# Kernel tuning notes

Measured on AMD Instinct MI355X. Metric: run time of the kernel, lower is better.

The kernel has to match this reference:

```python
import jax, jax.numpy as jnp
import numpy as np

B, T, D, K = 32, 2048, 1024, 31


def setup_inputs() -> dict:
    key = jax.random.key(0)
    ks = jax.random.split(key, 8)
    query = jax.random.normal(ks[0], (B, D), dtype=jnp.float32)
    memory = jax.random.normal(ks[1], (B, T, D), dtype=jnp.float32)
    prev_attn = jax.nn.softmax(jax.random.normal(ks[2], (B, T)), axis=-1).astype(jnp.float32)
    cum_attn = jax.random.uniform(ks[3], (B, T), dtype=jnp.float32)
    mask = jax.random.bernoulli(ks[4], 0.2, (B, T))
    mask = mask.at[:, 0].set(False)  # keep at least one valid position per row
    scale = 0.02
    Wq = jax.random.normal(ks[5], (D, D), dtype=jnp.float32) * scale    # torch Linear weight [out,in]
    Wm = jax.random.normal(ks[6], (D, D), dtype=jnp.float32) * scale
    k2 = jax.random.split(ks[7], 2)
    Wloc = jax.random.normal(k2[0], (D, 2, K), dtype=jnp.float32) * scale  # Conv1d weight [out_ch,in_ch,k]
    v = jax.random.normal(k2[1], (D,), dtype=jnp.float32) * scale          # Linear(d_model,1) weight squeezed
    return {"query": query, "memory": memory, "prev_attn": prev_attn,
            "cum_attn": cum_attn, "mask": mask,
            "Wq": Wq, "Wm": Wm, "Wloc": Wloc, "v": v}


def reference(query, memory, prev_attn, cum_attn, mask, Wq, Wm, Wloc, v):
    pad = Wloc.shape[-1] // 2
    # location features: [B,2,T] conv -> [B,D,T] -> [B,T,D]
    loc_in = jnp.stack([prev_attn, cum_attn], axis=1)
    loc = jax.lax.conv_general_dilated(
        loc_in, Wloc, window_strides=(1,), padding=[(pad, pad)],
        dimension_numbers=("NCW", "OIW", "NCW"))
    loc = jnp.transpose(loc, (0, 2, 1))                 # [B,T,D]
    q = (query @ Wq.T)[:, None, :]                      # [B,1,D]
    m = jnp.einsum("btd,ed->bte", memory, Wm)           # [B,T,D]
    e = jnp.einsum("btd,d->bt", jnp.tanh(q + m + loc), v)  # [B,T]
    e = jnp.where(mask, -jnp.inf, e)
    a = jax.nn.softmax(e, axis=1)                       # [B,T]
    ctx = jnp.einsum("bt,btd->bd", a, memory)           # [B,D]
    return ctx, a
```

## Files before the change

kernel.cpp:

```cpp
#include <hip/hip_runtime.h>
#include <math.h>

#define BATCH 32
#define T 2048
#define D 1024
#define KW 31
#define CPAD 15
#define KEXT 62
#define KTOT 1088
#define BM 256
#define BN 256
#define KSTEP 64
#define NK (KTOT / KSTEP)

typedef __bf16 bf16_8 __attribute__((ext_vector_type(8)));
typedef __bf16 bf16_4 __attribute__((ext_vector_type(4)));
typedef float  f32x4  __attribute__((ext_vector_type(4)));

__device__ __forceinline__ float tanh_fast(float x) {
    return 1.f - 2.f * __builtin_amdgcn_rcpf(__expf(2.f * x) + 1.f);
}

__device__ __forceinline__ void glds16(const void* gsrc, void* ldst) {
    __builtin_amdgcn_global_load_lds(
        (const __attribute__((address_space(1))) unsigned int*)gsrc,
        (__attribute__((address_space(3))) unsigned int*)ldst, 16, 0, 0);
}

#define VM6 asm volatile("s_waitcnt vmcnt(6)" ::: "memory")
#define VM4 asm volatile("s_waitcnt vmcnt(4)" ::: "memory")
#define VM0 asm volatile("s_waitcnt vmcnt(0)" ::: "memory")
#define BAR __builtin_amdgcn_s_barrier()
#define PRIO1 __builtin_amdgcn_s_setprio(1)
#define PRIO0 __builtin_amdgcn_s_setprio(0)

#define PREP_BLOCKS 17472
__global__ __launch_bounds__(256) void k_prep_all(
    const float* __restrict__ Wm, const float* __restrict__ Wloc,
    __bf16* __restrict__ Bext,
    const float* __restrict__ memory, __bf16* __restrict__ Amem,
    const float* __restrict__ prev, const float* __restrict__ cum,
    const float* __restrict__ query, const float* __restrict__ Wq,
    float* __restrict__ qout) {
    const int gb = blockIdx.x;
    if (gb < 4096) {
        const int nvec = BATCH * T * (D / 16);
        for (int idx = gb * 256 + threadIdx.x; idx < nvec; idx += 4096 * 256) {
            const int row = idx >> 6;
            const int c = (idx & 63) * 16;
            const float* src = memory + (size_t)row * D + c;
            const f32x4 a0 = *(const f32x4*)(src);
            const f32x4 a1 = *(const f32x4*)(src + 4);
            const f32x4 a2 = *(const f32x4*)(src + 8);
            const f32x4 a3 = *(const f32x4*)(src + 12);
            bf16_8 o0, o1;
            #pragma unroll
            for (int u = 0; u < 4; ++u) {
                o0[u] = (__bf16)a0[u]; o0[u + 4] = (__bf16)a1[u];
                o1[u] = (__bf16)a2[u]; o1[u + 4] = (__bf16)a3[u];
            }
            __bf16* dst = Amem + (size_t)row * KTOT + c;
            *(bf16_8*)(dst) = o0;
            *(bf16_8*)(dst + 8) = o1;
        }
    } else if (gb < 12288) {
        const int j = gb - 4096;
        const int xb = j & 255;
        const int b = j >> 8;
        const int w = threadIdx.x >> 6;
        const int lane = threadIdx.x & 63;
        const int d = xb * 4 + w;
        const float* qrow = query + (size_t)b * D;
        const float* wrow = Wq + (size_t)d * D;
        float s = 0.f;
        #pragma unroll
        for (int i = 0; i < D / 64; ++i) s += qrow[lane + i * 64] * wrow[lane + i * 64];
        #pragma unroll
        for (int off = 32; off > 0; off >>= 1) s += __shfl_down(s, off, 64);
        if (lane == 0) qout[(size_t)b * D + d] = s;
    } else if (gb < 16384) {
        const int idx = (gb - 12288) * 256 + threadIdx.x;
        const int row = idx >> 4;
        const int j0 = (idx & 15) * 4;
        const int b = row >> 11;
        const int t = row & (T - 1);
        bf16_4 o;
        #pragma unroll
        for (int u = 0; u < 4; ++u) {
            const int jj = j0 + u;
            float val = 0.f;
            if (jj < KEXT) {
                const int c = (jj >= KW) ? 1 : 0;
                const int kp = jj - c * KW;
                const int ts = t + kp - CPAD;
                if (ts >= 0 && ts < T)
                    val = (c ? cum : prev)[(size_t)b * T + ts];
            }
            o[u] = (__bf16)val;
        }
        *(bf16_4*)(Amem + (size_t)row * KTOT + D + j0) = o;
    } else {
        const int idx = (gb - 16384) * 256 + threadIdx.x;
        const int d = idx / (KTOT / 4);
        const int kk = (idx % (KTOT / 4)) * 4;
        bf16_4 o;
        #pragma unroll
        for (int u = 0; u < 4; ++u) {
            const int k = kk + u;
            float val = 0.f;
            if (k < D) val = Wm[(size_t)d * D + k];
            else {
                const int jj = k - D;
                if (jj < KEXT) {
                    const int c = (jj >= KW) ? 1 : 0;
                    const int kp = jj - c * KW;
                    val = Wloc[((size_t)d * 2 + c) * KW + kp];
                }
            }
            o[u] = (__bf16)val;
        }
        *(bf16_4*)(Bext + (size_t)d * KTOT + kk) = o;
    }
}

__global__ __launch_bounds__(512, 2) void k_gemm_e(
    const __bf16* __restrict__ Amem, const __bf16* __restrict__ Bext,
    const float* __restrict__ qv, const float* __restrict__ vvec,
    float* __restrict__ e_part) {
    __shared__ bf16_8 As[2][2048];
    __shared__ bf16_8 Bs[2][2048];

    const int t0 = blockIdx.x * BM;
    const int d0 = blockIdx.y * BN;
    const int b  = blockIdx.z;
    const int tid  = threadIdx.x;
    const int lane = tid & 63;
    const int w    = tid >> 6;
    const int wm   = w >> 2;
    const int wn   = w & 3;
    const int ml   = lane & 15;
    const int qk   = lane >> 4;

    f32x4 acc[8][4] = {};

    const __bf16* gA[2][2];
    const __bf16* gB[2][2];
    int sA[2][2], sB[2][2];
    #pragma unroll
    for (int h = 0; h < 2; ++h) {
        #pragma unroll
        for (int j = 0; j < 2; ++j) {
            const int idx = j * 8 + w;
            const int p = idx >> 1, kfa = idx & 1;
            const int mf = h * 4 + (p & 3) + (idx & 8);
            const int nf = h * 2 + (p & 1) + (p >> 1) * 4;
            gA[h][j] = Amem + ((size_t)b * T + t0 + mf * 16 + ml) * KTOT + kfa * 32 + qk * 8;
            sA[h][j] = (mf * 2 + kfa) * 64;
            gB[h][j] = Bext + (size_t)(d0 + nf * 16 + ml) * KTOT + kfa * 32 + qk * 8;
            sB[h][j] = (nf * 2 + kfa) * 64;
        }
    }

    bf16_8 areg[4][2];
    bf16_8 breg0[2][2], breg1[2][2];

    auto STG_A = [&](int h, int kcol, bf16_8* dst) {
        glds16(gA[h][0] + kcol, dst + sA[h][0]);
        glds16(gA[h][1] + kcol, dst + sA[h][1]);
    };
    auto STG_B = [&](int h, int kcol, bf16_8* dst) {
        glds16(gB[h][0] + kcol, dst + sB[h][0]);
        glds16(gB[h][1] + kcol, dst + sB[h][1]);
    };
    auto LDA = [&](const bf16_8* buf, int ih) {
        #pragma unroll
        for (int i = 0; i < 4; ++i)
            #pragma unroll
            for (int kf = 0; kf < 2; ++kf)
                areg[i][kf] = buf[((wm * 8 + ih * 4 + i) * 2 + kf) * 64 + lane];
    };
    auto LDB = [&](bf16_8 (&dst)[2][2], const bf16_8* buf, int jh) {
        #pragma unroll
        for (int j = 0; j < 2; ++j)
            #pragma unroll
            for (int kf = 0; kf < 2; ++kf)
                dst[j][kf] = buf[((wn * 4 + jh * 2 + j) * 2 + kf) * 64 + lane];
    };
    auto QMM = [&](bf16_8 (&bb)[2][2], int ih, int jh) {
        #pragma unroll
        for (int i = 0; i < 4; ++i)
            #pragma unroll
            for (int kf = 0; kf < 2; ++kf)
                #pragma unroll
                for (int j = 0; j < 2; ++j)
                    acc[ih * 4 + i][jh * 2 + j] = __builtin_amdgcn_mfma_f32_16x16x32_bf16(
                        areg[i][kf], bb[j][kf], acc[ih * 4 + i][jh * 2 + j], 0, 0, 0);
    };

    STG_A(0, 0, As[0]);
    STG_B(0, 0, Bs[0]);
    STG_B(1, 0, Bs[0]);
    STG_A(1, 0, As[0]);
    VM4;
    BAR;

    #pragma unroll 1
    for (int k = 0; k < NK; ++k) {
        const bf16_8* Ac = As[k & 1];
        const bf16_8* Bc = Bs[k & 1];
        bf16_8* An = As[(k + 1) & 1];
        bf16_8* Bn = Bs[(k + 1) & 1];
        const int c1 = ((k + 1 < NK) ? (k + 1) : 0) * KSTEP;
        LDA(Ac, 0);
        LDB(breg0, Bc, 0);
        STG_A(0, c1, An);
        STG_B(0, c1, Bn);
        BAR;
        PRIO1; QMM(breg0, 0, 0); PRIO0;
        VM6;
        BAR;
        LDB(breg1, Bc, 1);
        STG_B(1, c1, Bn);
        BAR;
        PRIO1; QMM(breg1, 0, 1); PRIO0;
        VM6;
        BAR;
        LDA(Ac, 1);
        STG_A(1, c1, An);
        BAR;
        PRIO1; QMM(breg0, 1, 0); PRIO0;
        BAR;
        PRIO1; QMM(breg1, 1, 1); PRIO0;
        VM4;
        BAR;
    }
    VM0;
    BAR;

    float qreg[4], vreg[4];
    #pragma unroll
    for (int jb = 0; jb < 4; ++jb) {
        const int d = d0 + wn * 64 + jb * 16 + ml;
        qreg[jb] = qv[(size_t)b * D + d];
        vreg[jb] = vvec[d];
    }
    float (*est)[256] = (float (*)[256])(&As[0][0]);
    #pragma unroll
    for (int ia = 0; ia < 8; ++ia) {
        #pragma unroll
        for (int r = 0; r < 4; ++r) {
            float s = 0.f;
            #pragma unroll
            for (int jb = 0; jb < 4; ++jb)
                s += tanh_fast(acc[ia][jb][r] + qreg[jb]) * vreg[jb];
            #pragma unroll
            for (int off = 8; off > 0; off >>= 1)
                s += __shfl_down(s, off, 16);
            if (ml == 0)
                est[wn][wm * 128 + ia * 16 + qk * 4 + r] = s;
        }
    }
    __syncthreads();
    if (tid < 256) {
        const float e = est[0][tid] + est[1][tid] + est[2][tid] + est[3][tid];
        e_part[((size_t)b * T + t0 + tid) * 4 + blockIdx.y] = e;
    }
}

__global__ __launch_bounds__(256) void k_softmax(const float* __restrict__ e_part,
                                                 const int* __restrict__ mask,
                                                 float* __restrict__ aout) {
    const int b = blockIdx.x;
    const int tid = threadIdx.x;
    __shared__ float red[256];
    float ev[8];
    float lmax = -INFINITY;
    #pragma unroll
    for (int i = 0; i < 8; ++i) {
        const int t = tid + i * 256;
        const f32x4 p4 = *(const f32x4*)(e_part + ((size_t)b * T + t) * 4);
        float s = p4[0] + p4[1] + p4[2] + p4[3];
        if (mask[(size_t)b * T + t] != 0) s = -INFINITY;
        ev[i] = s;
        lmax = fmaxf(lmax, s);
    }
    red[tid] = lmax; __syncthreads();
    for (int off = 128; off > 0; off >>= 1) {
        if (tid < off) red[tid] = fmaxf(red[tid], red[tid + off]);
        __syncthreads();
    }
    const float mx = red[0]; __syncthreads();
    float lsum = 0.f;
    #pragma unroll
    for (int i = 0; i < 8; ++i) {
        const float x = expf(ev[i] - mx);
        ev[i] = x;
        lsum += x;
    }
    red[tid] = lsum; __syncthreads();
    for (int off = 128; off > 0; off >>= 1) {
        if (tid < off) red[tid] += red[tid + off];
        __syncthreads();
    }
    const float inv = 1.f / red[0];
    #pragma unroll
    for (int i = 0; i < 8; ++i)
        aout[(size_t)b * T + tid + i * 256] = ev[i] * inv;
}

__global__ __launch_bounds__(256) void k_ctx_part(const __bf16* __restrict__ Amem,
                                                  const float* __restrict__ a,
                                                  float* __restrict__ ctx_part) {
    const int b = blockIdx.x;
    const int tc = blockIdx.y;
    const int th = threadIdx.x >> 7;
    const int cg = threadIdx.x & 127;
    const int d8 = cg * 8;
    __shared__ float red[128][8];
    float acc[8] = {};
    const int trow = tc * 64 + th * 32;
    const __bf16* mb = Amem + ((size_t)b * T + trow) * KTOT + d8;
    const float* ab = a + (size_t)b * T + trow;
    #pragma unroll 4
    for (int t = 0; t < 32; ++t) {
        const float wgt = ab[t];
        const bf16_8 m8 = *(const bf16_8*)(mb + (size_t)t * KTOT);
        #pragma unroll
        for (int u = 0; u < 8; ++u) acc[u] += wgt * (float)m8[u];
    }
    if (th == 1) {
        #pragma unroll
        for (int u = 0; u < 8; ++u) red[cg][u] = acc[u];
    }
    __syncthreads();
    if (th == 0) {
        f32x4 o0, o1;
        #pragma unroll
        for (int u = 0; u < 4; ++u) {
            o0[u] = acc[u] + red[cg][u];
            o1[u] = acc[u + 4] + red[cg][u + 4];
        }
        float* dst = ctx_part + ((size_t)(b * 32 + tc)) * D + d8;
        *(f32x4*)(dst) = o0;
        *(f32x4*)(dst + 4) = o1;
    }
}

__global__ __launch_bounds__(256) void k_ctx_red(const float* __restrict__ ctx_part,
                                                 float* __restrict__ ctx) {
    const int idx = blockIdx.x * 256 + threadIdx.x;
    const int b = idx >> 10, d = idx & 1023;
    float s = 0.f;
    #pragma unroll
    for (int tc = 0; tc < 32; ++tc) s += ctx_part[((size_t)(b * 32 + tc)) * D + d];
    ctx[idx] = s;
}

extern "C" void kernel_launch(void* const* d_in, const int* in_sizes, int n_in,
                              void* d_out, int out_size, void* d_ws, size_t ws_size,
                              hipStream_t stream) {
    const float* query  = (const float*)d_in[0];
    const float* memory = (const float*)d_in[1];
    const float* prev   = (const float*)d_in[2];
    const float* cum    = (const float*)d_in[3];
    const int*   mask   = (const int*)d_in[4];
    const float* Wq     = (const float*)d_in[5];
    const float* Wm     = (const float*)d_in[6];
    const float* Wloc   = (const float*)d_in[7];
    const float* v      = (const float*)d_in[8];

    float* out = (float*)d_out;
    float* ctx = out;
    float* a   = out + BATCH * D;

    char* ws = (char*)d_ws;
    float*  qv       = (float*)(ws + 0);
    float*  e_part   = (float*)(ws + 131072);
    float*  ctx_part = (float*)(ws + 4325376);
    __bf16* Bext     = (__bf16*)(ws + 8519680);
    __bf16* Amem     = (__bf16*)(ws + 10747904);

    k_prep_all<<<PREP_BLOCKS, 256, 0, stream>>>(Wm, Wloc, Bext, memory, Amem,
                                                prev, cum, query, Wq, qv);
    k_gemm_e<<<dim3(T / BM, D / BN, BATCH), 512, 0, stream>>>(Amem, Bext, qv, v, e_part);
    k_softmax<<<BATCH, 256, 0, stream>>>(e_part, mask, a);
    k_ctx_part<<<dim3(BATCH, 32), 256, 0, stream>>>(Amem, a, ctx_part);
    k_ctx_red<<<(BATCH * D) / 256, 256, 0, stream>>>(ctx_part, ctx);
}
```

Baseline: 618.1 us.

## Deepen GEMM prefetch to two stages and remap blocks across XCDs

```diff
diff --git a/kernel.cpp b/kernel.cpp
--- a/kernel.cpp
+++ b/kernel.cpp
@@ -27,8 +27,8 @@
         (__attribute__((address_space(3))) unsigned int*)ldst, 16, 0, 0);
 }
 
+#define VM8 asm volatile("s_waitcnt vmcnt(8)" ::: "memory")
 #define VM6 asm volatile("s_waitcnt vmcnt(6)" ::: "memory")
-#define VM4 asm volatile("s_waitcnt vmcnt(4)" ::: "memory")
 #define VM0 asm volatile("s_waitcnt vmcnt(0)" ::: "memory")
 #define BAR __builtin_amdgcn_s_barrier()
 #define PRIO1 __builtin_amdgcn_s_setprio(1)
@@ -130,9 +130,14 @@
     __shared__ bf16_8 As[2][2048];
     __shared__ bf16_8 Bs[2][2048];
 
-    const int t0 = blockIdx.x * BM;
-    const int d0 = blockIdx.y * BN;
-    const int b  = blockIdx.z;
+    const int hw = blockIdx.x + 8 * (blockIdx.y + 4 * blockIdx.z);
+    const int logical = (hw & 7) * 128 + (hw >> 3);
+    const int b  = logical >> 5;
+    const int r  = logical & 31;
+    const int t0 = (r >> 2) * BM;
+    const int dt = r & 3;
+    const int d0 = dt * BN;
+
     const int tid  = threadIdx.x;
     const int lane = tid & 63;
     const int w    = tid >> 6;
@@ -201,20 +206,21 @@
     STG_B(0, 0, Bs[0]);
     STG_B(1, 0, Bs[0]);
     STG_A(1, 0, As[0]);
-    VM4;
+    STG_A(0, KSTEP, As[1]);
+    STG_B(0, KSTEP, Bs[1]);
+    VM8;
     BAR;
 
     #pragma unroll 1
     for (int k = 0; k < NK; ++k) {
-        const bf16_8* Ac = As[k & 1];
-        const bf16_8* Bc = Bs[k & 1];
+        bf16_8* Ac = As[k & 1];
+        bf16_8* Bc = Bs[k & 1];
         bf16_8* An = As[(k + 1) & 1];
         bf16_8* Bn = Bs[(k + 1) & 1];
         const int c1 = ((k + 1 < NK) ? (k + 1) : 0) * KSTEP;
+        const int c2 = ((k + 2 < NK) ? (k + 2) : 0) * KSTEP;
         LDA(Ac, 0);
         LDB(breg0, Bc, 0);
-        STG_A(0, c1, An);
-        STG_B(0, c1, Bn);
         BAR;
         PRIO1; QMM(breg0, 0, 0); PRIO0;
         VM6;
@@ -230,8 +236,10 @@
         BAR;
         PRIO1; QMM(breg0, 1, 0); PRIO0;
         BAR;
+        STG_A(0, c2, Ac);
+        STG_B(0, c2, Bc);
         PRIO1; QMM(breg1, 1, 1); PRIO0;
-        VM4;
+        VM8;
         BAR;
     }
     VM0;
@@ -248,22 +256,22 @@
     #pragma unroll
     for (int ia = 0; ia < 8; ++ia) {
         #pragma unroll
-        for (int r = 0; r < 4; ++r) {
+        for (int r2 = 0; r2 < 4; ++r2) {
             float s = 0.f;
             #pragma unroll
             for (int jb = 0; jb < 4; ++jb)
-                s += tanh_fast(acc[ia][jb][r] + qreg[jb]) * vreg[jb];
+                s += tanh_fast(acc[ia][jb][r2] + qreg[jb]) * vreg[jb];
             #pragma unroll
             for (int off = 8; off > 0; off >>= 1)
                 s += __shfl_down(s, off, 16);
             if (ml == 0)
-                est[wn][wm * 128 + ia * 16 + qk * 4 + r] = s;
+                est[wn][wm * 128 + ia * 16 + qk * 4 + r2] = s;
         }
     }
     __syncthreads();
     if (tid < 256) {
         const float e = est[0][tid] + est[1][tid] + est[2][tid] + est[3][tid];
-        e_part[((size_t)b * T + t0 + tid) * 4 + blockIdx.y] = e;
+        e_part[((size_t)b * T + t0 + tid) * 4 + dt] = e;
     }
 }
 
```

New measurement: 640.0 us. 3.5% more time.
